# Kernel tuning notes

Measured on AMD Instinct MI355X. Metric: run time of the kernel, lower is better.

## Reference

```python
import jax, jax.numpy as jnp
import numpy as np

B, T, H = 2048, 128, 128
K1, K2 = 16, 15  # hardcoded input_size / input_size1 in the torch module


def setup_inputs() -> dict:
    key = jax.random.key(0)
    ks = jax.random.split(key, 8)
    s = 0.05
    return {
        "X": jax.random.normal(ks[0], (B, T - 1, K2), jnp.float32),
        "y_prev": jax.random.normal(ks[1], (B, T - 1), jnp.float32),
        # shared attention linear: in_features = 2H + T-1, out_features = 1
        "Wa": jax.random.normal(ks[2], (2 * H + T - 1, 1), jnp.float32) * s,
        "ba": jnp.zeros((1,), jnp.float32),
        # LSTM 1 (input K1=16): torch gate order i,f,g,o stacked in 4H
        "Wih1": jax.random.normal(ks[3], (4 * H, K1), jnp.float32) * s,
        "Whh1": jax.random.normal(ks[4], (4 * H, H), jnp.float32) * s,
        "bih1": jnp.zeros((4 * H,), jnp.float32),
        "bhh1": jnp.zeros((4 * H,), jnp.float32),
        # LSTM 2 (input K2=15)
        "Wih2": jax.random.normal(ks[5], (4 * H, K2), jnp.float32) * s,
        "Whh2": jax.random.normal(ks[6], (4 * H, H), jnp.float32) * s,
        "bih2": jnp.zeros((4 * H,), jnp.float32),
        "bhh2": jnp.zeros((4 * H,), jnp.float32),
    }


def _lstm_step(x, h, c, Wih, Whh, bih, bhh):
    g = x @ Wih.T + h @ Whh.T + (bih + bhh)
    i, f, gg, o = jnp.split(g, 4, axis=-1)
    c = jax.nn.sigmoid(f) * c + jax.nn.sigmoid(i) * jnp.tanh(gg)
    h = jax.nn.sigmoid(o) * jnp.tanh(c)
    return h, c


def reference(X, y_prev, Wa, ba, Wih1, Whh1, bih1, bhh1, Wih2, Whh2, bih2, bhh2):
    Bn = X.shape[0]
    Hn = Whh1.shape[1]
    x_y = jnp.concatenate([X, y_prev[..., None]], axis=2)  # (B, T-1, K1)
    mm = X * y_prev[..., None]                              # (B, T-1, K2)
    xy_f = jnp.swapaxes(x_y, 1, 2)  # (B, K1, T-1) per-feature time series
    mm_f = jnp.swapaxes(mm, 1, 2)   # (B, K2, T-1)

    def attn(h, c, feats, K):
        # cat([h rep K, c rep K, feats], dim=2) @ Wa + ba -> softmax over features
        z = jnp.concatenate([
            jnp.broadcast_to(h[:, None, :], (Bn, K, Hn)),
            jnp.broadcast_to(c[:, None, :], (Bn, K, Hn)),
            feats], axis=2)                      # (B, K, 2H + T-1)
        e = (z @ Wa)[..., 0] + ba[0]             # (B, K)
        return jax.nn.softmax(e, axis=1)

    def step(carry, inp):
        h1, c1, h2, c2 = carry
        xyt, mmt = inp  # (B, K1), (B, K2)
        a1 = attn(h1, c1, xy_f, K1)
        xt1 = a1 * xyt
        h1, c1 = _lstm_step(xt1, h1, c1, Wih1, Whh1, bih1, bhh1)
        a2 = attn(h2, c2, mm_f, K2)
        xt2 = a2 * mmt
        h2, c2 = _lstm_step(xt2, h2, c2, Wih2, Whh2, bih2, bhh2)
        return (h1, c1, h2, c2), (xt1, jnp.concatenate([h1, h2], axis=-1))

    z0 = jnp.zeros((Bn, Hn), X.dtype)
    xs = (jnp.swapaxes(x_y, 0, 1), jnp.swapaxes(mm, 0, 1))  # time-major for scan
    _, (Xt, Xe) = jax.lax.scan(step, (z0, z0, z0, z0), xs)
    X_tilde = jnp.swapaxes(Xt, 0, 1)    # (B, T-1, K1)
    X_encoded = jnp.swapaxes(Xe, 0, 1)  # (B, T-1, 2H)
    return X_tilde, X_encoded
```

## Files before the change

kernel.cpp:

```cpp
#include <hip/hip_runtime.h>
#include <hip/hip_bf16.h>

#define TSTEPS 127
#define HDIM   128
#define NB     16
#define NBATCH 2048

typedef __attribute__((ext_vector_type(8))) short bfrag;
typedef __attribute__((ext_vector_type(4))) float f32x4;

static __device__ __forceinline__ unsigned short f2bf(float f) {
  union { float f; unsigned u; } v; v.f = f;
  unsigned r = (v.u + 0x7FFFu + ((v.u >> 16) & 1u)) >> 16;
  return (unsigned short)r;
}
static __device__ __forceinline__ unsigned short f2bf_fast(float f) {
  unsigned r;
  asm("v_cvt_pk_bf16_f32 %0, %1, 0" : "=v"(r) : "v"(f));
  return (unsigned short)r;
}

static __device__ __forceinline__ float tanh_p(float x) {
  x = fminf(2.0f, fmaxf(-2.0f, x));
  const float t = x * x;
  float p = fmaf(0.00282f, t, -0.0281139f);
  p = fmaf(p, t, 0.1176519f);
  p = fmaf(p, t, -0.3307639f);
  p = fmaf(p, t, 1.0f);
  return x * p;
}
static __device__ __forceinline__ float sigm_p(float x) {
  x = fminf(4.0f, fmaxf(-4.0f, x));
  const float t = x * x;
  float p = fmaf(1.10156e-5f, t, -4.3928e-4f);
  p = fmaf(p, t, 7.3532e-3f);
  p = fmaf(p, t, -0.08269098f);
  p = fmaf(p, t, 1.0f);
  return fmaf(x * p, 0.25f, 0.5f);
}

__global__ __launch_bounds__(512, 2)
void enc_kernel(const float* __restrict__ X, const float* __restrict__ yprev,
                const float* __restrict__ Wa,
                const float* __restrict__ Wih1, const float* __restrict__ Whh1,
                const float* __restrict__ bih1, const float* __restrict__ bhh1,
                const float* __restrict__ Wih2, const float* __restrict__ Whh2,
                const float* __restrict__ bih2, const float* __restrict__ bhh2,
                float* __restrict__ out)
{
  const int tid  = threadIdx.x;
  const int wv   = tid >> 6;
  const int lane = tid & 63;
  const int l15  = lane & 15;
  const int lg   = lane >> 4;
  const int lstm  = blockIdx.x >> 7;
  const int btile = blockIdx.x & 127;

  const float* Wih = lstm ? Wih2 : Wih1;
  const float* Whh = lstm ? Whh2 : Whh1;
  const float* bih = lstm ? bih2 : bih1;
  const float* bhh = lstm ? bhh2 : bhh1;
  const int Kin = lstm ? 15 : 16;

  __shared__ __align__(16) unsigned short h_lds[2][NB * HDIM];
  __shared__ __align__(16) unsigned short xt_lds[2][NB * 40];

  bfrag wb[4][4];
  bfrag wi[4];
  float bias[4];
  #pragma unroll
  for (int gt = 0; gt < 4; ++gt) {
    const int row = (gt * 8 + wv) * 16 + l15;
    const float* wr = Whh + row * HDIM;
    #pragma unroll
    for (int ks = 0; ks < 4; ++ks) {
      const int k0 = ks * 32 + lg * 8;
      bfrag v;
      #pragma unroll
      for (int e = 0; e < 8; ++e) v[e] = (short)f2bf(wr[k0 + e]);
      wb[gt][ks] = v;
    }
    bfrag v;
    #pragma unroll
    for (int e = 0; e < 8; ++e) {
      const int k = lg * 8 + e;
      v[e] = (k < Kin) ? (short)f2bf(Wih[row * Kin + k]) : (short)0;
    }
    wi[gt] = v;
    bias[gt] = bih[row] + bhh[row];
  }

  float a_bk = 0.0f;
  const int bloc = (tid >> 4) & 15;
  const int kf   = tid & 15;
  const size_t bg = (size_t)btile * NB + bloc;
  if (tid < 256) {
    float s = -1e30f;
    if (kf < Kin) {
      s = 0.0f;
      const float* xrow = X + bg * TSTEPS * 15;
      const float* yrow = yprev + bg * TSTEPS;
      for (int t = 0; t < TSTEPS; ++t) {
        const float wa = Wa[256 + t];
        float feat;
        if (lstm == 0) feat = (kf < 15) ? xrow[t * 15 + kf] : yrow[t];
        else           feat = xrow[t * 15 + kf] * yrow[t];
        s += feat * wa;
      }
    }
    float mx = s;
    #pragma unroll
    for (int m = 1; m < 16; m <<= 1) mx = fmaxf(mx, __shfl_xor(mx, m));
    const float e = __expf(s - mx);
    float sum = e;
    #pragma unroll
    for (int m = 1; m < 16; m <<= 1) sum += __shfl_xor(sum, m);
    a_bk = e / sum;
  }

  for (int i = tid; i < 2 * NB * HDIM; i += 512) ((unsigned short*)h_lds)[i] = 0;
  for (int i = tid; i < 2 * NB * 40;   i += 512) ((unsigned short*)xt_lds)[i] = 0;
  __syncthreads();

  const size_t XT_TOTAL = (size_t)NBATCH * TSTEPS * 16;
  const int u = wv * 16 + l15;
  float* pH[4];
  #pragma unroll
  for (int r = 0; r < 4; ++r) {
    const int b = lg * 4 + r;
    const size_t bgr = (size_t)btile * NB + b;
    pH[r] = out + XT_TOTAL + bgr * (TSTEPS * 256) + (size_t)lstm * 128 + u;
  }
  float* pXT = out + bg * (TSTEPS * 16) + kf;
  const float* pX = X + bg * (TSTEPS * 15) + kf;
  const float* pY = yprev + bg * TSTEPS;

  float xv = 0.f, yv = 0.f;
  if (tid < 256) {
    yv = pY[0];
    if (kf < 15) xv = pX[0];
    float feat;
    if (lstm == 0) feat = (kf < 15) ? xv : yv;
    else           feat = (kf < 15) ? xv * yv : 0.0f;
    const float xt = a_bk * feat;
    xt_lds[0][bloc * 40 + kf] = f2bf(xt);
    if (lstm == 0) pXT[0] = xt;
    yv = pY[1];
    if (kf < 15) xv = pX[15];
  }
  __syncthreads();

  float cr[4] = {0.f, 0.f, 0.f, 0.f};

  #pragma unroll 2
  for (int t = 0; t < TSTEPS; ++t) {
    bfrag ah[4], ax;
    #pragma unroll
    for (int ks = 0; ks < 4; ++ks) {
      const int idx = (l15 * HDIM + ks * 32 + lg * 8) ^ (l15 << 3);
      ah[ks] = *(const bfrag*)&h_lds[(t + 1) & 1][idx];
    }
    ax = *(const bfrag*)&xt_lds[t & 1][l15 * 40 + lg * 8];

    f32x4 acc[4];
    #pragma unroll
    for (int gt = 0; gt < 4; ++gt) {
      f32x4 a = {bias[gt], bias[gt], bias[gt], bias[gt]};
      #pragma unroll
      for (int ks = 0; ks < 4; ++ks)
        a = __builtin_amdgcn_mfma_f32_16x16x32_bf16(ah[ks], wb[gt][ks], a, 0, 0, 0);
      a = __builtin_amdgcn_mfma_f32_16x16x32_bf16(ax, wi[gt], a, 0, 0, 0);
      acc[gt] = a;
    }

    #pragma unroll
    for (int r = 0; r < 4; ++r) {
      const float ig = sigm_p(acc[0][r]);
      const float fg = sigm_p(acc[1][r]);
      const float gg = tanh_p(acc[2][r]);
      const float og = sigm_p(acc[3][r]);
      const float c = fg * cr[r] + ig * gg;
      cr[r] = c;
      const float h = og * tanh_p(c);
      const int b = lg * 4 + r;
      h_lds[t & 1][(b * HDIM + u) ^ ((b & 15) << 3)] = f2bf_fast(h);
      *pH[r] = h;
      pH[r] += 256;
    }

    if (tid < 256 && t < TSTEPS - 1) {
      float feat;
      if (lstm == 0) feat = (kf < 15) ? xv : yv;
      else           feat = (kf < 15) ? xv * yv : 0.0f;
      const float xt = a_bk * feat;
      xt_lds[(t + 1) & 1][bloc * 40 + kf] = f2bf_fast(xt);
      if (lstm == 0) pXT[(size_t)(t + 1) * 16] = xt;
      if (t < TSTEPS - 2) {
        yv = pY[t + 2];
        if (kf < 15) xv = pX[(size_t)(t + 2) * 15];
      }
    }

    asm volatile("s_waitcnt lgkmcnt(0)" ::: "memory");
    __builtin_amdgcn_s_barrier();
    __builtin_amdgcn_sched_barrier(0);
  }
}

extern "C" void kernel_launch(void* const* d_in, const int* in_sizes, int n_in,
                              void* d_out, int out_size, void* d_ws, size_t ws_size,
                              hipStream_t stream) {
  const float* X    = (const float*)d_in[0];
  const float* yp   = (const float*)d_in[1];
  const float* Wa   = (const float*)d_in[2];
  const float* Wih1 = (const float*)d_in[4];
  const float* Whh1 = (const float*)d_in[5];
  const float* bih1 = (const float*)d_in[6];
  const float* bhh1 = (const float*)d_in[7];
  const float* Wih2 = (const float*)d_in[8];
  const float* Whh2 = (const float*)d_in[9];
  const float* bih2 = (const float*)d_in[10];
  const float* bhh2 = (const float*)d_in[11];
  float* out = (float*)d_out;

  enc_kernel<<<dim3(256), dim3(512), 0, stream>>>(
      X, yp, Wa, Wih1, Whh1, bih1, bhh1, Wih2, Whh2, bih2, bhh2, out);
}
```

Before: 165.3 us.

## Run both LSTMs in one 1024-thread block with 8-row batch tiles

Each block now runs 16 waves: eight for LSTM1 and eight for LSTM2, both on an 8-batch tile, instead of one LSTM over 16 batches per 512-thread block. Each 16-row MFMA tile holds the 8 real rows duplicated, so every lane computes gate nonlinearities for 2 rows instead of 4. This shortens the per-step elementwise tail on the serial recurrence. The cost is half-wasted MFMA throughput, duplicated LDS writes, and one barrier shared by 16 waves.

```diff
diff --git a/kernel.cpp b/kernel.cpp
--- a/kernel.cpp
+++ b/kernel.cpp
@@ -3,7 +3,8 @@
 
 #define TSTEPS 127
 #define HDIM   128
-#define NB     16
+#define NB     8
+#define NBROW  16
 #define NBATCH 2048
 
 typedef __attribute__((ext_vector_type(8))) short bfrag;
@@ -39,7 +40,7 @@
   return fmaf(x * p, 0.25f, 0.5f);
 }
 
-__global__ __launch_bounds__(512, 2)
+__global__ __launch_bounds__(1024, 1)
 void enc_kernel(const float* __restrict__ X, const float* __restrict__ yprev,
                 const float* __restrict__ Wa,
                 const float* __restrict__ Wih1, const float* __restrict__ Whh1,
@@ -53,8 +54,9 @@
   const int lane = tid & 63;
   const int l15  = lane & 15;
   const int lg   = lane >> 4;
-  const int lstm  = blockIdx.x >> 7;
-  const int btile = blockIdx.x & 127;
+  const int lstm = wv >> 3;
+  const int w8   = wv & 7;
+  const int btile = blockIdx.x;
 
   const float* Wih = lstm ? Wih2 : Wih1;
   const float* Whh = lstm ? Whh2 : Whh1;
@@ -62,15 +64,15 @@
   const float* bhh = lstm ? bhh2 : bhh1;
   const int Kin = lstm ? 15 : 16;
 
-  __shared__ __align__(16) unsigned short h_lds[2][NB * HDIM];
-  __shared__ __align__(16) unsigned short xt_lds[2][NB * 40];
+  __shared__ __align__(16) unsigned short h_lds[2][2][NBROW * HDIM];
+  __shared__ __align__(16) unsigned short xt_lds[2][2][NBROW * 40];
 
   bfrag wb[4][4];
   bfrag wi[4];
   float bias[4];
   #pragma unroll
   for (int gt = 0; gt < 4; ++gt) {
-    const int row = (gt * 8 + wv) * 16 + l15;
+    const int row = (gt * 8 + w8) * 16 + l15;
     const float* wr = Whh + row * HDIM;
     #pragma unroll
     for (int ks = 0; ks < 4; ++ks) {
@@ -91,20 +93,22 @@
   }
 
   float a_bk = 0.0f;
-  const int bloc = (tid >> 4) & 15;
+  const int al   = tid >> 7;
+  const int bloc = (tid >> 4) & 7;
   const int kf   = tid & 15;
+  const int KinA = al ? 15 : 16;
   const size_t bg = (size_t)btile * NB + bloc;
   if (tid < 256) {
     float s = -1e30f;
-    if (kf < Kin) {
+    if (kf < KinA) {
       s = 0.0f;
       const float* xrow = X + bg * TSTEPS * 15;
       const float* yrow = yprev + bg * TSTEPS;
       for (int t = 0; t < TSTEPS; ++t) {
         const float wa = Wa[256 + t];
         float feat;
-        if (lstm == 0) feat = (kf < 15) ? xrow[t * 15 + kf] : yrow[t];
-        else           feat = xrow[t * 15 + kf] * yrow[t];
+        if (al == 0) feat = (kf < 15) ? xrow[t * 15 + kf] : yrow[t];
+        else         feat = xrow[t * 15 + kf] * yrow[t];
         s += feat * wa;
       }
     }
@@ -118,19 +122,17 @@
     a_bk = e / sum;
   }
 
-  for (int i = tid; i < 2 * NB * HDIM; i += 512) ((unsigned short*)h_lds)[i] = 0;
-  for (int i = tid; i < 2 * NB * 40;   i += 512) ((unsigned short*)xt_lds)[i] = 0;
+  for (int i = tid; i < 2 * 2 * NBROW * HDIM; i += 1024) ((unsigned short*)h_lds)[i] = 0;
+  for (int i = tid; i < 2 * 2 * NBROW * 40;   i += 1024) ((unsigned short*)xt_lds)[i] = 0;
   __syncthreads();
 
+  const int row0 = (lg & 1) * 4 + (lg >> 1) * 2;
+  const int row1 = row0 + 1;
+  const int u = w8 * 16 + l15;
+
   const size_t XT_TOTAL = (size_t)NBATCH * TSTEPS * 16;
-  const int u = wv * 16 + l15;
-  float* pH[4];
-  #pragma unroll
-  for (int r = 0; r < 4; ++r) {
-    const int b = lg * 4 + r;
-    const size_t bgr = (size_t)btile * NB + b;
-    pH[r] = out + XT_TOTAL + bgr * (TSTEPS * 256) + (size_t)lstm * 128 + u;
-  }
+  float* pH0 = out + XT_TOTAL + ((size_t)btile * NB + row0) * (TSTEPS * 256) + (size_t)lstm * 128 + u;
+  float* pH1 = out + XT_TOTAL + ((size_t)btile * NB + row1) * (TSTEPS * 256) + (size_t)lstm * 128 + u;
   float* pXT = out + bg * (TSTEPS * 16) + kf;
   const float* pX = X + bg * (TSTEPS * 15) + kf;
   const float* pY = yprev + bg * TSTEPS;
@@ -140,17 +142,19 @@
     yv = pY[0];
     if (kf < 15) xv = pX[0];
     float feat;
-    if (lstm == 0) feat = (kf < 15) ? xv : yv;
-    else           feat = (kf < 15) ? xv * yv : 0.0f;
+    if (al == 0) feat = (kf < 15) ? xv : yv;
+    else         feat = (kf < 15) ? xv * yv : 0.0f;
     const float xt = a_bk * feat;
-    xt_lds[0][bloc * 40 + kf] = f2bf(xt);
-    if (lstm == 0) pXT[0] = xt;
+    const unsigned short xtb = f2bf(xt);
+    xt_lds[al][0][bloc * 40 + kf] = xtb;
+    xt_lds[al][0][(bloc + 8) * 40 + kf] = xtb;
+    if (al == 0) pXT[0] = xt;
     yv = pY[1];
     if (kf < 15) xv = pX[15];
   }
   __syncthreads();
 
-  float cr[4] = {0.f, 0.f, 0.f, 0.f};
+  float cr0 = 0.f, cr1 = 0.f;
 
   #pragma unroll 2
   for (int t = 0; t < TSTEPS; ++t) {
@@ -158,9 +162,9 @@
     #pragma unroll
     for (int ks = 0; ks < 4; ++ks) {
       const int idx = (l15 * HDIM + ks * 32 + lg * 8) ^ (l15 << 3);
-      ah[ks] = *(const bfrag*)&h_lds[(t + 1) & 1][idx];
-    }
-    ax = *(const bfrag*)&xt_lds[t & 1][l15 * 40 + lg * 8];
+      ah[ks] = *(const bfrag*)&h_lds[lstm][(t + 1) & 1][idx];
+    }
+    ax = *(const bfrag*)&xt_lds[lstm][t & 1][l15 * 40 + lg * 8];
 
     f32x4 acc[4];
     #pragma unroll
@@ -173,28 +177,43 @@
       acc[gt] = a;
     }
 
-    #pragma unroll
-    for (int r = 0; r < 4; ++r) {
-      const float ig = sigm_p(acc[0][r]);
-      const float fg = sigm_p(acc[1][r]);
-      const float gg = tanh_p(acc[2][r]);
-      const float og = sigm_p(acc[3][r]);
-      const float c = fg * cr[r] + ig * gg;
-      cr[r] = c;
+    float g0[4], g1[4];
+    #pragma unroll
+    for (int gt = 0; gt < 4; ++gt) {
+      g0[gt] = (lg < 2) ? acc[gt][0] : acc[gt][2];
+      g1[gt] = (lg < 2) ? acc[gt][1] : acc[gt][3];
+    }
+
+    {
+      const float ig = sigm_p(g0[0]), fg = sigm_p(g0[1]);
+      const float gg = tanh_p(g0[2]), og = sigm_p(g0[3]);
+      const float c = fg * cr0 + ig * gg;  cr0 = c;
       const float h = og * tanh_p(c);
-      const int b = lg * 4 + r;
-      h_lds[t & 1][(b * HDIM + u) ^ ((b & 15) << 3)] = f2bf_fast(h);
-      *pH[r] = h;
-      pH[r] += 256;
+      const unsigned short hb = f2bf_fast(h);
+      h_lds[lstm][t & 1][(row0 * HDIM + u) ^ (row0 << 3)] = hb;
+      h_lds[lstm][t & 1][((row0 + 8) * HDIM + u) ^ ((row0 + 8) << 3)] = hb;
+      *pH0 = h;  pH0 += 256;
+    }
+    {
+      const float ig = sigm_p(g1[0]), fg = sigm_p(g1[1]);
+      const float gg = tanh_p(g1[2]), og = sigm_p(g1[3]);
+      const float c = fg * cr1 + ig * gg;  cr1 = c;
+      const float h = og * tanh_p(c);
+      const unsigned short hb = f2bf_fast(h);
+      h_lds[lstm][t & 1][(row1 * HDIM + u) ^ (row1 << 3)] = hb;
+      h_lds[lstm][t & 1][((row1 + 8) * HDIM + u) ^ ((row1 + 8) << 3)] = hb;
+      *pH1 = h;  pH1 += 256;
     }
 
     if (tid < 256 && t < TSTEPS - 1) {
       float feat;
-      if (lstm == 0) feat = (kf < 15) ? xv : yv;
-      else           feat = (kf < 15) ? xv * yv : 0.0f;
+      if (al == 0) feat = (kf < 15) ? xv : yv;
+      else         feat = (kf < 15) ? xv * yv : 0.0f;
       const float xt = a_bk * feat;
-      xt_lds[(t + 1) & 1][bloc * 40 + kf] = f2bf_fast(xt);
-      if (lstm == 0) pXT[(size_t)(t + 1) * 16] = xt;
+      const unsigned short xtb = f2bf_fast(xt);
+      xt_lds[al][(t + 1) & 1][bloc * 40 + kf] = xtb;
+      xt_lds[al][(t + 1) & 1][(bloc + 8) * 40 + kf] = xtb;
+      if (al == 0) pXT[(size_t)(t + 1) * 16] = xt;
       if (t < TSTEPS - 2) {
         yv = pY[t + 2];
         if (kf < 15) xv = pX[(size_t)(t + 2) * 15];
@@ -223,6 +242,6 @@
   const float* bhh2 = (const float*)d_in[11];
   float* out = (float*)d_out;
 
-  enc_kernel<<<dim3(256), dim3(512), 0, stream>>>(
+  enc_kernel<<<dim3(256), dim3(1024), 0, stream>>>(
       X, yp, Wa, Wih1, Whh1, bih1, bhh1, Wih2, Whh2, bih2, bhh2, out);
 }
```

Result: slower. 524.3 us (+217.2%).

## Split batch tile into two half-sets and ping-pong MFMA with epilogue

Applied to the files above, without the earlier changes.

Splits each block's 16-row batch tile into two sets of 8 rows whose recurrences are interleaved. The MFMA for one set overlaps the gate epilogue of the other, hiding the serial dependency inside each timestep. Each set's h and xt rows are duplicated into both halves of the 16-row MFMA tile, so half the MFMA work is redundant. Occupancy hint drops from 2 to 1 block per CU.

```diff
diff --git a/kernel.cpp b/kernel.cpp
--- a/kernel.cpp
+++ b/kernel.cpp
@@ -3,7 +3,6 @@
 
 #define TSTEPS 127
 #define HDIM   128
-#define NB     16
 #define NBATCH 2048
 
 typedef __attribute__((ext_vector_type(8))) short bfrag;
@@ -39,7 +38,13 @@
   return fmaf(x * p, 0.25f, 0.5f);
 }
 
-__global__ __launch_bounds__(512, 2)
+#define BARRIER() do {                                         \
+    asm volatile("s_waitcnt lgkmcnt(0)" ::: "memory");         \
+    __builtin_amdgcn_s_barrier();                              \
+    __builtin_amdgcn_sched_barrier(0);                         \
+  } while (0)
+
+__global__ __launch_bounds__(512, 1)
 void enc_kernel(const float* __restrict__ X, const float* __restrict__ yprev,
                 const float* __restrict__ Wa,
                 const float* __restrict__ Wih1, const float* __restrict__ Whh1,
@@ -62,8 +67,8 @@
   const float* bhh = lstm ? bhh2 : bhh1;
   const int Kin = lstm ? 15 : 16;
 
-  __shared__ __align__(16) unsigned short h_lds[2][NB * HDIM];
-  __shared__ __align__(16) unsigned short xt_lds[2][NB * 40];
+  __shared__ __align__(16) unsigned short hA[16 * HDIM], hB[16 * HDIM];
+  __shared__ __align__(16) unsigned short xtA[16 * 40], xtB[16 * 40];
 
   bfrag wb[4][4];
   bfrag wi[4];
@@ -93,7 +98,8 @@
   float a_bk = 0.0f;
   const int bloc = (tid >> 4) & 15;
   const int kf   = tid & 15;
-  const size_t bg = (size_t)btile * NB + bloc;
+  const int sset = bloc >> 3;
+  const size_t bg = (size_t)btile * 16 + bloc;
   if (tid < 256) {
     float s = -1e30f;
     if (kf < Kin) {
@@ -118,51 +124,58 @@
     a_bk = e / sum;
   }
 
-  for (int i = tid; i < 2 * NB * HDIM; i += 512) ((unsigned short*)h_lds)[i] = 0;
-  for (int i = tid; i < 2 * NB * 40;   i += 512) ((unsigned short*)xt_lds)[i] = 0;
+  for (int i = tid; i < 16 * HDIM; i += 512) { hA[i] = 0; hB[i] = 0; }
+  for (int i = tid; i < 16 * 40;   i += 512) { xtA[i] = 0; xtB[i] = 0; }
   __syncthreads();
 
+  const int row0 = (lg & 1) * 4 + (lg >> 1) * 2;
+  const int row1 = row0 + 1;
+  const int u = wv * 16 + l15;
+
   const size_t XT_TOTAL = (size_t)NBATCH * TSTEPS * 16;
-  const int u = wv * 16 + l15;
-  float* pH[4];
-  #pragma unroll
-  for (int r = 0; r < 4; ++r) {
-    const int b = lg * 4 + r;
-    const size_t bgr = (size_t)btile * NB + b;
-    pH[r] = out + XT_TOTAL + bgr * (TSTEPS * 256) + (size_t)lstm * 128 + u;
-  }
-  float* pXT = out + bg * (TSTEPS * 16) + kf;
-  const float* pX = X + bg * (TSTEPS * 15) + kf;
-  const float* pY = yprev + bg * TSTEPS;
-
+  float* pHA0 = out + XT_TOTAL + ((size_t)btile * 16 + 0 + row0) * (TSTEPS * 256) + (size_t)lstm * 128 + u;
+  float* pHA1 = out + XT_TOTAL + ((size_t)btile * 16 + 0 + row1) * (TSTEPS * 256) + (size_t)lstm * 128 + u;
+  float* pHB0 = out + XT_TOTAL + ((size_t)btile * 16 + 8 + row0) * (TSTEPS * 256) + (size_t)lstm * 128 + u;
+  float* pHB1 = out + XT_TOTAL + ((size_t)btile * 16 + 8 + row1) * (TSTEPS * 256) + (size_t)lstm * 128 + u;
+  float* pXTc = out + bg * (TSTEPS * 16) + kf;
+  const float* pXn = X + bg * (TSTEPS * 15) + kf;
+  const float* pYn = yprev + bg * TSTEPS;
   float xv = 0.f, yv = 0.f;
+
   if (tid < 256) {
-    yv = pY[0];
-    if (kf < 15) xv = pX[0];
-    float feat;
-    if (lstm == 0) feat = (kf < 15) ? xv : yv;
-    else           feat = (kf < 15) ? xv * yv : 0.0f;
-    const float xt = a_bk * feat;
-    xt_lds[0][bloc * 40 + kf] = f2bf(xt);
-    if (lstm == 0) pXT[0] = xt;
-    yv = pY[1];
-    if (kf < 15) xv = pX[15];
-  }
-  __syncthreads();
-
-  float cr[4] = {0.f, 0.f, 0.f, 0.f};
-
-  #pragma unroll 2
-  for (int t = 0; t < TSTEPS; ++t) {
+    yv = pYn[0];  pYn += 1;
+    if (kf < 15) xv = pXn[0];
+    pXn += 15;
+  }
+
+  auto STAGE = [&](int setS, int ts) {
+    if (tid < 256 && sset == setS) {
+      float feat;
+      if (lstm == 0) feat = (kf < 15) ? xv : yv;
+      else           feat = (kf < 15) ? xv * yv : 0.0f;
+      const float xt = a_bk * feat;
+      const unsigned short xtb = f2bf_fast(xt);
+      unsigned short* xb = setS ? xtB : xtA;
+      const int bl = bloc & 7;
+      xb[bl * 40 + kf] = xtb;
+      xb[(bl + 8) * 40 + kf] = xtb;
+      if (lstm == 0) { *pXTc = xt; pXTc += 16; }
+      if (ts < TSTEPS - 1) {
+        yv = *pYn;  pYn += 1;
+        if (kf < 15) xv = *pXn;
+        pXn += 15;
+      }
+    }
+  };
+
+  auto MFMA = [&](const unsigned short* hbuf, const unsigned short* xbuf, f32x4* acc) {
     bfrag ah[4], ax;
     #pragma unroll
     for (int ks = 0; ks < 4; ++ks) {
       const int idx = (l15 * HDIM + ks * 32 + lg * 8) ^ (l15 << 3);
-      ah[ks] = *(const bfrag*)&h_lds[(t + 1) & 1][idx];
-    }
-    ax = *(const bfrag*)&xt_lds[t & 1][l15 * 40 + lg * 8];
-
-    f32x4 acc[4];
+      ah[ks] = *(const bfrag*)&hbuf[idx];
+    }
+    ax = *(const bfrag*)&xbuf[l15 * 40 + lg * 8];
     #pragma unroll
     for (int gt = 0; gt < 4; ++gt) {
       f32x4 a = {bias[gt], bias[gt], bias[gt], bias[gt]};
@@ -172,39 +185,61 @@
       a = __builtin_amdgcn_mfma_f32_16x16x32_bf16(ax, wi[gt], a, 0, 0, 0);
       acc[gt] = a;
     }
-
-    #pragma unroll
-    for (int r = 0; r < 4; ++r) {
-      const float ig = sigm_p(acc[0][r]);
-      const float fg = sigm_p(acc[1][r]);
-      const float gg = tanh_p(acc[2][r]);
-      const float og = sigm_p(acc[3][r]);
-      const float c = fg * cr[r] + ig * gg;
-      cr[r] = c;
+  };
+
+  auto EPI = [&](const f32x4* acc, unsigned short* hbuf,
+                 float*& p0, float*& p1, float& c0, float& c1) {
+    float g0[4], g1[4];
+    #pragma unroll
+    for (int gt = 0; gt < 4; ++gt) {
+      g0[gt] = (lg < 2) ? acc[gt][0] : acc[gt][2];
+      g1[gt] = (lg < 2) ? acc[gt][1] : acc[gt][3];
+    }
+    {
+      const float ig = sigm_p(g0[0]), fg = sigm_p(g0[1]);
+      const float gg = tanh_p(g0[2]), og = sigm_p(g0[3]);
+      const float c = fg * c0 + ig * gg;  c0 = c;
       const float h = og * tanh_p(c);
-      const int b = lg * 4 + r;
-      h_lds[t & 1][(b * HDIM + u) ^ ((b & 15) << 3)] = f2bf_fast(h);
-      *pH[r] = h;
-      pH[r] += 256;
-    }
-
-    if (tid < 256 && t < TSTEPS - 1) {
-      float feat;
-      if (lstm == 0) feat = (kf < 15) ? xv : yv;
-      else           feat = (kf < 15) ? xv * yv : 0.0f;
-      const float xt = a_bk * feat;
-      xt_lds[(t + 1) & 1][bloc * 40 + kf] = f2bf_fast(xt);
-      if (lstm == 0) pXT[(size_t)(t + 1) * 16] = xt;
-      if (t < TSTEPS - 2) {
-        yv = pY[t + 2];
-        if (kf < 15) xv = pX[(size_t)(t + 2) * 15];
-      }
-    }
-
-    asm volatile("s_waitcnt lgkmcnt(0)" ::: "memory");
-    __builtin_amdgcn_s_barrier();
-    __builtin_amdgcn_sched_barrier(0);
-  }
+      const unsigned short hb = f2bf_fast(h);
+      hbuf[(row0 * HDIM + u) ^ (row0 << 3)] = hb;
+      hbuf[((row0 + 8) * HDIM + u) ^ ((row0 + 8) << 3)] = hb;
+      *p0 = h;  p0 += 256;
+    }
+    {
+      const float ig = sigm_p(g1[0]), fg = sigm_p(g1[1]);
+      const float gg = tanh_p(g1[2]), og = sigm_p(g1[3]);
+      const float c = fg * c1 + ig * gg;  c1 = c;
+      const float h = og * tanh_p(c);
+      const unsigned short hb = f2bf_fast(h);
+      hbuf[(row1 * HDIM + u) ^ (row1 << 3)] = hb;
+      hbuf[((row1 + 8) * HDIM + u) ^ ((row1 + 8) << 3)] = hb;
+      *p1 = h;  p1 += 256;
+    }
+  };
+
+  STAGE(0, 0);
+  __syncthreads();
+
+  f32x4 accA[4], accB[4];
+  float crA0 = 0.f, crA1 = 0.f, crB0 = 0.f, crB1 = 0.f;
+
+  MFMA(hA, xtA, accA);
+  STAGE(1, 0);
+  BARRIER();
+
+  for (int t = 0; t < TSTEPS - 1; ++t) {
+    MFMA(hB, xtB, accB);
+    EPI(accA, hA, pHA0, pHA1, crA0, crA1);
+    STAGE(0, t + 1);
+    BARRIER();
+    MFMA(hA, xtA, accA);
+    EPI(accB, hB, pHB0, pHB1, crB0, crB1);
+    STAGE(1, t + 1);
+    BARRIER();
+  }
+  MFMA(hB, xtB, accB);
+  EPI(accA, hA, pHA0, pHA1, crA0, crA1);
+  EPI(accB, hB, pHB0, pHB1, crB0, crB1);
 }
 
 extern "C" void kernel_launch(void* const* d_in, const int* in_sizes, int n_in,
```

Measured after the change: 216.8 us. +31.2%, slower.
